# Performance work log

Measured on AMD Instinct MI355X. Metric: run time of the kernel, lower is better.

The kernel has to match this reference:

```python
import jax, jax.numpy as jnp
import numpy as np

B, H, W, C = 8, 56, 56, 384
HEADS = 12
HD = C // HEADS          # 32 head dim
WS = 7                   # window size
SS = 3                   # shift size
N = WS * WS              # 49 tokens per window
HID = int(C * 4.0)       # 1536 mlp hidden
NW = (H // WS) * (W // WS)  # 64 windows per image
EPS = 1e-5


def _relative_position_index(ws):
    coords = np.stack(np.meshgrid(np.arange(ws), np.arange(ws), indexing='ij'))
    cf = coords.reshape(2, -1)
    rel = (cf[:, :, None] - cf[:, None, :]).transpose(1, 2, 0)
    rel[:, :, 0] += ws - 1
    rel[:, :, 1] += ws - 1
    rel[:, :, 0] *= 2 * ws - 1
    return rel.sum(-1).astype(np.int32)  # [N, N]

REL_IDX = _relative_position_index(WS)


def _swin_shift_mask(hh, ww, ws, ss):
    # standard Swin shift mask: label 9 regions, windows with mixed labels get -100
    img = np.zeros((hh, ww), dtype=np.float32)
    cnt = 0
    for hs in (slice(0, -ws), slice(-ws, -ss), slice(-ss, None)):
        for wsl in (slice(0, -ws), slice(-ws, -ss), slice(-ss, None)):
            img[hs, wsl] = cnt
            cnt += 1
    wins = img.reshape(hh // ws, ws, ww // ws, ws).transpose(0, 2, 1, 3).reshape(-1, ws * ws)
    diff = wins[:, None, :] - wins[:, :, None]
    return np.where(diff != 0, -100.0, 0.0).astype(np.float32)  # [nW, N, N]


def setup_inputs() -> dict:
    key = jax.random.key(0)
    ks = jax.random.split(key, 8)
    s = 0.02
    return {
        'x': jax.random.normal(ks[0], (B, H, W, C), jnp.float32),
        'attention_mask': jnp.asarray(_swin_shift_mask(H, W, WS, SS)),
        'qkv_w': jax.random.normal(ks[1], (C, 3 * C), jnp.float32) * s,
        'qkv_b': jnp.zeros((3 * C,), jnp.float32),
        'proj_w': jax.random.normal(ks[2], (C, C), jnp.float32) * s,
        'proj_b': jnp.zeros((C,), jnp.float32),
        'rpb_table': jax.random.normal(ks[3], ((2 * WS - 1) * (2 * WS - 1), HEADS), jnp.float32) * s,
        'norm1_g': jnp.ones((C,), jnp.float32),
        'norm1_b': jnp.zeros((C,), jnp.float32),
        'norm2_g': jnp.ones((C,), jnp.float32),
        'norm2_b': jnp.zeros((C,), jnp.float32),
        'fc1_w': jax.random.normal(ks[4], (C, HID), jnp.float32) * s,
        'fc1_b': jnp.zeros((HID,), jnp.float32),
        'fc2_w': jax.random.normal(ks[5], (HID, C), jnp.float32) * s,
        'fc2_b': jnp.zeros((C,), jnp.float32),
    }


def _ln(x, g, b):
    mu = jnp.mean(x, axis=-1, keepdims=True)
    var = jnp.mean(jnp.square(x - mu), axis=-1, keepdims=True)
    return (x - mu) / jnp.sqrt(var + EPS) * g + b


def reference(x, attention_mask, qkv_w, qkv_b, proj_w, proj_b, rpb_table,
              norm1_g, norm1_b, norm2_g, norm2_b, fc1_w, fc1_b, fc2_w, fc2_b):
    b = x.shape[0]
    nh, nw = H // WS, W // WS
    shortcut = x.reshape(b, H * W, C)

    h = _ln(x, norm1_g, norm1_b)
    # cyclic shift (H,W divisible by WS -> no padding needed)
    h = jnp.roll(h, (-SS, -SS), axis=(1, 2))
    # window partition -> [b*nW, N, C]
    win = h.reshape(b, nh, WS, nw, WS, C).transpose(0, 1, 3, 2, 4, 5).reshape(-1, N, C)

    qkv = (win @ qkv_w + qkv_b).reshape(-1, N, 3, HEADS, HD).transpose(2, 0, 3, 1, 4)
    q, k, v = qkv[0] * (HD ** -0.5), qkv[1], qkv[2]  # each [b*nW, heads, N, HD]

    attn = jnp.einsum('bhnd,bhmd->bhnm', q, k)  # [b*nW, heads, N, N]
    bias = rpb_table[REL_IDX.reshape(-1)].reshape(N, N, HEADS).transpose(2, 0, 1)
    attn = attn + bias[None]
    # additive shift mask per window
    attn = attn.reshape(b, NW, HEADS, N, N) + attention_mask[None, :, None]
    attn = jax.nn.softmax(attn.reshape(-1, HEADS, N, N), axis=-1)

    out = jnp.einsum('bhnm,bhmd->bhnd', attn, v).transpose(0, 2, 1, 3).reshape(-1, N, C)
    out = out @ proj_w + proj_b
    # window reverse
    out = out.reshape(b, nh, nw, WS, WS, C).transpose(0, 1, 3, 2, 4, 5).reshape(b, H, W, C)
    out = jnp.roll(out, (SS, SS), axis=(1, 2)).reshape(b, H * W, C)

    xr = shortcut + out
    m = _ln(xr.reshape(b, H * W, C), norm2_g, norm2_b)
    m = jax.nn.gelu(m @ fc1_w + fc1_b, approximate=False) @ fc2_w + fc2_b
    xr = xr + m
    return xr.reshape(b, H, W, C)
```

## Files before the change

### kernel.cpp

```cpp
#include <hip/hip_runtime.h>
#include <hip/hip_bf16.h>
#include <math.h>

#define BD 8
#define HH 56
#define WW 56
#define CC 384
#define HEADS 12
#define HD 32
#define WS 7
#define SS 3
#define NTOK 49
#define NWIN 64
#define TOKENS (BD*HH*WW)
#define HID 1536
#define TPI (HH*WW)

typedef __attribute__((ext_vector_type(8))) short bf16x8;
typedef __attribute__((ext_vector_type(4))) float f32x4;

__device__ __forceinline__ unsigned short f2bf(float f) {
    unsigned int u = __float_as_uint(f);
    unsigned int r = (u + 0x7FFFu + ((u >> 16) & 1u)) >> 16;
    return (unsigned short)r;
}
__device__ __forceinline__ unsigned short f2bf_fast(float v) {
    unsigned int w;
    asm("v_cvt_pk_bf16_f32 %0, %1, %2" : "=v"(w) : "v"(v), "v"(v));
    return (unsigned short)w;
}
__device__ __forceinline__ float bf2f(unsigned short h) {
    return __uint_as_float(((unsigned int)h) << 16);
}
__device__ __forceinline__ void gload16(const void* g, void* l) {
    __builtin_amdgcn_global_load_lds((const __attribute__((address_space(1))) unsigned int*)g,
                                     (__attribute__((address_space(3))) unsigned int*)l, 16, 0, 0);
}
__device__ __forceinline__ float fgelu(float x) {
    float x2 = x * x;
    float y  = x * fmaf(0.03567740814f, x2, 0.7978845608f);
    float e  = exp2f(y * 2.8853900818f);
    float r  = __builtin_amdgcn_rcpf(e + 1.0f);
    return x - x * r;
}
__device__ __forceinline__ int xcd_swz(int lid, int nwg) {
    int xcd = lid & 7, pos = lid >> 3;
    int q = nwg >> 3, r = nwg & 7;
    return (xcd < r ? xcd * (q + 1) : r * (q + 1) + (xcd - r) * q) + pos;
}

__global__ __launch_bounds__(256)
void wprep(const float* __restrict__ W, unsigned short* __restrict__ Th, int K, int N)
{
    __shared__ float t[32][33];
    int n0 = blockIdx.x * 32, k0 = blockIdx.y * 32;
    int c = threadIdx.x & 31, r = threadIdx.x >> 5;
    #pragma unroll
    for (int rr = 0; rr < 32; rr += 8)
        t[r + rr][c] = W[(size_t)(k0 + r + rr) * N + n0 + c];
    __syncthreads();
    #pragma unroll
    for (int rr = 0; rr < 32; rr += 8) {
        int i = r + rr;
        Th[(size_t)(n0 + i) * K + k0 + c] = f2bf(t[c][i]);
    }
}

__global__ __launch_bounds__(256)
void bias_prep(const float* __restrict__ rpb, float* __restrict__ Bias)
{
    int e = blockIdx.x * 256 + threadIdx.x;
    int wtq = e / 49152;
    int hr  = e - wtq * 49152;
    int h   = hr >> 12;
    int rem = hr & 4095;
    int jt = rem >> 10, it = (rem >> 8) & 3, lane = (rem >> 2) & 63, reg = rem & 3;
    int j = jt * 16 + ((lane >> 4) << 2) + reg;
    int i = it * 16 + (lane & 15);
    float val;
    if (j >= NTOK) val = -1e30f;
    else if (i >= NTOK) val = 0.0f;
    else {
        int ti = i / 7, tj = i - ti * 7, yj = j / 7, xj = j - yj * 7;
        float b = rpb[((ti - yj + 6) * 13 + (tj - xj + 6)) * HEADS + h];
        int wh7 = wtq >> 1, ww7 = wtq & 1;
        int lhi = wh7 ? (ti < 4 ? 1 : 2) : 0, lhj = wh7 ? (yj < 4 ? 1 : 2) : 0;
        int lwi = ww7 ? (tj < 4 ? 1 : 2) : 0, lwj = ww7 ? (xj < 4 ? 1 : 2) : 0;
        if (lhi != lhj || lwi != lwj) b -= 100.0f;
        val = b * 5.65685424949238f;
    }
    Bias[e] = val;
}

template<bool SHIFT>
__global__ __launch_bounds__(128)
void ln_kernel(const float* __restrict__ in, const float* __restrict__ g,
               const float* __restrict__ beta, unsigned short* __restrict__ oh)
{
    int m = blockIdx.x;
    const float* src;
    size_t dbase = (size_t)m * CC;
    if (SHIFT) {
        int b  = m / (NWIN * NTOK);
        int rr = m % (NWIN * NTOK);
        int w  = rr / NTOK;
        int t  = rr % NTOK;
        int wh = w >> 3, ww = w & 7;
        int ti = t / 7,  tj = t - (t / 7) * 7;
        int hh = wh * WS + ti + SS;  if (hh >= HH) hh -= HH;
        int w2 = ww * WS + tj + SS;  if (w2 >= WW) w2 -= WW;
        src = in + ((size_t)b * TPI + hh * WW + w2) * CC;
    } else {
        src = in + (size_t)m * CC;
    }
    int tid = threadIdx.x;
    float v0 = src[tid], v1 = src[tid + 128], v2 = src[tid + 256];
    float s  = v0 + v1 + v2;
    float ss = v0*v0 + v1*v1 + v2*v2;
    #pragma unroll
    for (int off = 32; off > 0; off >>= 1) {
        s  += __shfl_down(s, off);
        ss += __shfl_down(ss, off);
    }
    __shared__ float red[4];
    int wid = tid >> 6, lane = tid & 63;
    if (lane == 0) { red[wid] = s; red[wid + 2] = ss; }
    __syncthreads();
    float tot   = red[0] + red[1];
    float totss = red[2] + red[3];
    float mu   = tot * (1.0f / CC);
    float var  = totss * (1.0f / CC) - mu * mu;
    float rstd = rsqrtf(var + 1e-5f);
    #pragma unroll
    for (int e = 0; e < 3; ++e) {
        int idx = tid + e * 128;
        float v = (e == 0 ? v0 : (e == 1 ? v1 : v2));
        float y = (v - mu) * rstd * g[idx] + beta[idx];
        oh[dbase + idx] = f2bf_fast(y);
    }
}

#define EPI_QKV  0
#define EPI_GELU 1
#define EPI_PROJ 2
#define EPI_FC2  3

template<int EPI>
__global__ __launch_bounds__(512)
void gemm_mfma(const unsigned short* __restrict__ Ah, const unsigned short* __restrict__ Bh,
               const float* __restrict__ bias, const float* __restrict__ extra,
               float* __restrict__ outf, unsigned short* __restrict__ outh,
               int M, int N, int K)
{
    __shared__ unsigned short lds[2][128][32];

    int nwg = gridDim.x * gridDim.y;
    int wid = xcd_swz(blockIdx.y * gridDim.x + blockIdx.x, nwg);
    int nblk = wid % gridDim.x;
    int mblk = wid / gridDim.x;

    int tid  = threadIdx.x;
    int lane = tid & 63;
    int wave = tid >> 6;
    int wr = wave >> 2;
    int wc = wave & 3;
    int m0 = mblk * 128, n0 = nblk * 128;

    int lrow = lane >> 2;
    int ps   = lane & 3;
    int kslot = lane >> 4;
    int rA    = lane & 15;

    const unsigned short* gsrc[2];
    unsigned short* dsts[2];
    #pragma unroll
    for (int s = 0; s < 2; ++s) {
        int seg = wave * 2 + s;
        int bf = seg >> 3, c = seg & 7;
        const unsigned short* gb = (bf == 0) ? Ah : Bh;
        int r0 = (bf == 0) ? m0 : n0;
        int row = c * 16 + lrow;
        int ks = ps ^ ((row >> 1) & 3);
        gsrc[s] = gb + (size_t)(r0 + row) * K + ks * 8;
        dsts[s] = &lds[bf][c * 16][0];
    }

    f32x4 acc[4][2];
    #pragma unroll
    for (int i = 0; i < 4; ++i)
        #pragma unroll
        for (int j = 0; j < 2; ++j)
            acc[i][j] = (f32x4){0.f, 0.f, 0.f, 0.f};

    for (int k0 = 0; k0 < K; k0 += 32) {
        #pragma unroll
        for (int s = 0; s < 2; ++s)
            gload16(gsrc[s] + k0, dsts[s]);
        __syncthreads();

        bf16x8 ah[4], bh[2];
        #pragma unroll
        for (int f = 0; f < 4; ++f) {
            int row = wr * 64 + f * 16 + rA;
            int p = (kslot ^ ((row >> 1) & 3)) * 8;
            ah[f] = *(const bf16x8*)&lds[0][row][p];
        }
        #pragma unroll
        for (int f = 0; f < 2; ++f) {
            int col = wc * 32 + f * 16 + rA;
            int pb = (kslot ^ ((col >> 1) & 3)) * 8;
            bh[f] = *(const bf16x8*)&lds[1][col][pb];
        }
        #pragma unroll
        for (int i = 0; i < 4; ++i)
            #pragma unroll
            for (int j = 0; j < 2; ++j)
                acc[i][j] = __builtin_amdgcn_mfma_f32_16x16x32_bf16(ah[i], bh[j], acc[i][j], 0, 0, 0);
        __syncthreads();
    }

    int cn = lane & 15;
    int rb = (lane >> 4) * 4;
    float bj[2];
    #pragma unroll
    for (int j = 0; j < 2; ++j) bj[j] = bias[n0 + wc * 32 + j * 16 + cn];
    int ncol = n0 + wc * 32 + cn;

    #pragma unroll
    for (int i = 0; i < 4; ++i) {
        #pragma unroll
        for (int r = 0; r < 4; ++r) {
            int mg = m0 + wr * 64 + i * 16 + rb + r;
            if (EPI == EPI_PROJ) {
                int b  = mg / (NWIN * NTOK);
                int rr = mg % (NWIN * NTOK);
                int w  = rr / NTOK;
                int t  = rr % NTOK;
                int wh = w >> 3, ww = w & 7;
                int ti = t / 7,  tj = t - (t / 7) * 7;
                int hh = wh * WS + ti + SS;  if (hh >= HH) hh -= HH;
                int w2 = ww * WS + tj + SS;  if (w2 >= WW) w2 -= WW;
                size_t pix = (size_t)b * TPI + hh * WW + w2;
                const float* xin = extra + pix * CC + ncol;
                float* xo = outf + pix * CC + ncol;
                #pragma unroll
                for (int j = 0; j < 2; ++j) xo[j * 16] = xin[j * 16] + acc[i][j][r] + bj[j];
            } else {
                const float* xi = extra + (size_t)mg * N + ncol;
                float* xo = outf + (size_t)mg * N + ncol;
                #pragma unroll
                for (int j = 0; j < 2; ++j) xo[j * 16] = xi[j * 16] + acc[i][j][r] + bj[j];
            }
        }
    }
}

template<int EPI>
__global__ __launch_bounds__(512)
void gemm_mfma256(const unsigned short* __restrict__ Ah, const unsigned short* __restrict__ Bh,
                  const float* __restrict__ bias,
                  float* __restrict__ outf, unsigned short* __restrict__ outh,
                  int M, int N, int K)
{
    __shared__ unsigned short ldsA[2][256][32];
    __shared__ unsigned short ldsB[2][128][32];

    int nwg = gridDim.x * gridDim.y;
    int wid = xcd_swz(blockIdx.y * gridDim.x + blockIdx.x, nwg);
    int nblk = wid % gridDim.x;
    int mblk = wid / gridDim.x;

    int tid  = threadIdx.x;
    int lane = tid & 63;
    int wave = tid >> 6;
    int wr = wave >> 1;
    int wc = wave & 1;
    int m0 = mblk * 256, n0 = nblk * 128;

    int lrow = lane >> 2;
    int ps   = lane & 3;
    int kslot = lane >> 4;
    int rA    = lane & 15;

    const unsigned short* gsrc[3];
    unsigned short* dst0[3];
    unsigned short* dst1[3];
    #pragma unroll
    for (int s = 0; s < 3; ++s) {
        int seg = wave * 3 + s;
        const unsigned short* gb;
        unsigned short *l0, *l1;
        int c, r0;
        if (seg < 16) { gb = Ah; c = seg;      r0 = m0; l0 = &ldsA[0][c * 16][0]; l1 = &ldsA[1][c * 16][0]; }
        else          { gb = Bh; c = seg - 16; r0 = n0; l0 = &ldsB[0][c * 16][0]; l1 = &ldsB[1][c * 16][0]; }
        int row = c * 16 + lrow;
        int ks = ps ^ ((row >> 1) & 3);
        gsrc[s] = gb + (size_t)(r0 + row) * K + ks * 8;
        dst0[s] = l0; dst1[s] = l1;
    }

    f32x4 acc[4][4];
    #pragma unroll
    for (int i = 0; i < 4; ++i)
        #pragma unroll
        for (int j = 0; j < 4; ++j)
            acc[i][j] = (f32x4){0.f, 0.f, 0.f, 0.f};

    for (int k0 = 0; k0 < K; k0 += 64) {
        #pragma unroll
        for (int s = 0; s < 3; ++s)
            gload16(gsrc[s] + k0, dst0[s]);
        #pragma unroll
        for (int s = 0; s < 3; ++s)
            gload16(gsrc[s] + k0 + 32, dst1[s]);
        __syncthreads();

        #pragma unroll
        for (int h = 0; h < 2; ++h) {
            bf16x8 ah[4], bh[4];
            #pragma unroll
            for (int f = 0; f < 4; ++f) {
                int row = wr * 64 + f * 16 + rA;
                int p = (kslot ^ ((row >> 1) & 3)) * 8;
                ah[f] = *(const bf16x8*)&ldsA[h][row][p];
                int col = wc * 64 + f * 16 + rA;
                int pb = (kslot ^ ((col >> 1) & 3)) * 8;
                bh[f] = *(const bf16x8*)&ldsB[h][col][pb];
            }
            #pragma unroll
            for (int i = 0; i < 4; ++i)
                #pragma unroll
                for (int j = 0; j < 4; ++j)
                    acc[i][j] = __builtin_amdgcn_mfma_f32_16x16x32_bf16(ah[i], bh[j], acc[i][j], 0, 0, 0);
        }
        __syncthreads();
    }

    int cn = lane & 15;
    int rb = (lane >> 4) * 4;
    float bj[4];
    #pragma unroll
    for (int j = 0; j < 4; ++j) bj[j] = bias[n0 + wc * 64 + j * 16 + cn];
    int ncol = n0 + wc * 64 + cn;

    #pragma unroll
    for (int i = 0; i < 4; ++i) {
        #pragma unroll
        for (int r = 0; r < 4; ++r) {
            int mg = m0 + wr * 64 + i * 16 + rb + r;
            if (EPI == EPI_QKV) {
                unsigned short* orow = outh + (size_t)mg * N + ncol;
                #pragma unroll
                for (int j = 0; j < 4; ++j) orow[j * 16] = f2bf_fast(acc[i][j][r] + bj[j]);
            } else {
                unsigned short* orow = outh + (size_t)mg * N + ncol;
                #pragma unroll
                for (int j = 0; j < 4; ++j)
                    orow[j * 16] = f2bf_fast(fgelu(acc[i][j][r] + bj[j]));
            }
        }
    }
}

__global__ __launch_bounds__(256)
void attn3(const unsigned short* __restrict__ QKVb, const float* __restrict__ Bias,
           unsigned short* __restrict__ outh, int win0)
{
    int wave = threadIdx.x >> 6, lane = threadIdx.x & 63;
    int unit = blockIdx.x * 4 + wave;
    int head = unit % HEADS;
    int winl = unit / HEADS;
    int wing = win0 + winl;
    int wl   = wing & (NWIN - 1);
    int wt   = (((wl >> 3) == 7) << 1) | ((wl & 7) == 7);
    int qbase = winl * NTOK;
    size_t obase = (size_t)wing * NTOK;

    __shared__ __align__(16) unsigned short Pl_all[4][64][64];
    __shared__ __align__(16) unsigned short Vt_all[4][2048];
    unsigned short (*Pl)[64] = Pl_all[wave];
    unsigned short* Vt = Vt_all[wave];

    int l15 = lane & 15, g = lane >> 4;

    for (int idx = lane; idx < 480; idx += 64) {
        int d = idx & 31, t = 49 + (idx >> 5);
        Vt[d * 64 + (((t >> 3) ^ (d & 7)) << 3) + (t & 7)] = 0;
    }
    for (int idx = lane; idx < 196; idx += 64) {
        int t = idx >> 2, c = idx & 3;
        bf16x8 v = *(const bf16x8*)(QKVb + (size_t)(qbase + t) * 1152 + 768 + head * HD + c * 8);
        int tb = t >> 3, tl = t & 7;
        #pragma unroll
        for (int e = 0; e < 8; ++e) {
            int d = c * 8 + e;
            Vt[d * 64 + ((tb ^ e) << 3) + tl] = (unsigned short)v[e];
        }
    }

    bf16x8 kf[4], qf[4];
    #pragma unroll
    for (int t = 0; t < 4; ++t) {
        int rr = t * 16 + l15; if (rr > NTOK - 1) rr = NTOK - 1;
        const unsigned short* base = QKVb + (size_t)(qbase + rr) * 1152 + head * HD + g * 8;
        qf[t] = *(const bf16x8*)base;
        kf[t] = *(const bf16x8*)(base + 384);
    }

    const float* bb = Bias + (((size_t)wt * HEADS + head) << 12);
    f32x4 acc[4][4];
    #pragma unroll
    for (int jt = 0; jt < 4; ++jt)
        #pragma unroll
        for (int it = 0; it < 4; ++it) {
            f32x4 c = *(const f32x4*)(bb + ((jt * 4 + it) * 64 + lane) * 4);
            acc[jt][it] = __builtin_amdgcn_mfma_f32_16x16x32_bf16(kf[jt], qf[it], c, 0, 0, 0);
        }

    const float K1 = 0.25503488f;
    #pragma unroll
    for (int jt = 0; jt < 4; ++jt)
        #pragma unroll
        for (int it = 0; it < 4; ++it)
            #pragma unroll
            for (int r = 0; r < 4; ++r)
                acc[jt][it][r] = exp2f(acc[jt][it][r] * K1);

    #pragma unroll
    for (int it = 0; it < 4; ++it) {
        float s = 0.0f;
        #pragma unroll
        for (int jt = 0; jt < 4; ++jt)
            s += (acc[jt][it][0] + acc[jt][it][1]) + (acc[jt][it][2] + acc[jt][it][3]);
        s += __shfl_xor(s, 16);
        s += __shfl_xor(s, 32);
        float inv = 1.0f / s;
        int i  = it * 16 + l15;
        int sw = (i & 7) << 3;
        #pragma unroll
        for (int jt = 0; jt < 4; ++jt) {
            float a0 = acc[jt][it][0] * inv, a1 = acc[jt][it][1] * inv;
            float a2 = acc[jt][it][2] * inv, a3 = acc[jt][it][3] * inv;
            unsigned int w0, w1;
            asm("v_cvt_pk_bf16_f32 %0, %1, %2" : "=v"(w0) : "v"(a0), "v"(a1));
            asm("v_cvt_pk_bf16_f32 %0, %1, %2" : "=v"(w1) : "v"(a2), "v"(a3));
            int js = (jt * 16 + g * 4) ^ sw;
            *(unsigned int*)&Pl[i][js]     = w0;
            *(unsigned int*)&Pl[i][js + 2] = w1;
        }
    }

    bf16x8 vf[2][2];
    #pragma unroll
    for (int dt = 0; dt < 2; ++dt)
        #pragma unroll
        for (int kc = 0; kc < 2; ++kc) {
            int d = dt * 16 + l15;
            vf[dt][kc] = *(const bf16x8*)&Vt[d * 64 + (((kc * 4 + g) ^ (d & 7)) << 3)];
        }
    f32x4 oacc[4][2];
    #pragma unroll
    for (int it = 0; it < 4; ++it)
        #pragma unroll
        for (int dt = 0; dt < 2; ++dt)
            oacc[it][dt] = (f32x4){0.f, 0.f, 0.f, 0.f};

    #pragma unroll
    for (int it = 0; it < 4; ++it) {
        int i  = it * 16 + l15;
        int sw = (i & 7) << 3;
        #pragma unroll
        for (int kc = 0; kc < 2; ++kc) {
            int js = (kc * 32 + g * 8) ^ sw;
            bf16x8 pf = *(const bf16x8*)&Pl[i][js];
            #pragma unroll
            for (int dt = 0; dt < 2; ++dt)
                oacc[it][dt] = __builtin_amdgcn_mfma_f32_16x16x32_bf16(pf, vf[dt][kc], oacc[it][dt], 0, 0, 0);
        }
    }

    #pragma unroll
    for (int it = 0; it < 4; ++it) {
        #pragma unroll
        for (int r = 0; r < 4; ++r) {
            int i = it * 16 + g * 4 + r;
            if (i < NTOK) {
                unsigned short* orow = outh + (obase + i) * CC + head * HD;
                orow[l15]      = f2bf_fast(oacc[it][0][r]);
                orow[16 + l15] = f2bf_fast(oacc[it][1][r]);
            }
        }
    }
}

extern "C" void kernel_launch(void* const* d_in, const int* in_sizes, int n_in,
                              void* d_out, int out_size, void* d_ws, size_t ws_size,
                              hipStream_t stream)
{
    const float* x      = (const float*)d_in[0];
    const float* qkv_w  = (const float*)d_in[2];
    const float* qkv_b  = (const float*)d_in[3];
    const float* proj_w = (const float*)d_in[4];
    const float* proj_b = (const float*)d_in[5];
    const float* rpb    = (const float*)d_in[6];
    const float* n1g    = (const float*)d_in[7];
    const float* n1b    = (const float*)d_in[8];
    const float* n2g    = (const float*)d_in[9];
    const float* n2b    = (const float*)d_in[10];
    const float* fc1w   = (const float*)d_in[11];
    const float* fc1b   = (const float*)d_in[12];
    const float* fc2w   = (const float*)d_in[13];
    const float* fc2b   = (const float*)d_in[14];

    float* xr = (float*)d_out;

    unsigned short* p = (unsigned short*)d_ws;
    unsigned short* Wqh = p; p += 442368;
    unsigned short* Wph = p; p += 147456;
    unsigned short* W1h = p; p += 589824;
    unsigned short* W2h = p; p += 589824;
    unsigned short* ABh = p; p += (size_t)TOKENS * CC;
    float* Bias = (float*)p;
    unsigned short* region = (unsigned short*)(Bias + 196608);
    unsigned short* Hbuf = region;

    const size_t FIXED = 23592960;
    size_t R = (ws_size > FIXED) ? ws_size - FIXED : 0;
    int gq = 2;
    if (R >= (size_t)8 * TPI * 1152 * 2)      gq = 8;
    else if (R >= (size_t)4 * TPI * 1152 * 2) gq = 4;
    int gh = 2;
    if (R >= (size_t)8 * TPI * HID * 2)      gh = 8;
    else if (R >= (size_t)4 * TPI * HID * 2) gh = 4;

    unsigned short* QKVb = region;

    bias_prep<<<768, 256, 0, stream>>>(rpb, Bias);
    wprep<<<dim3(1152/32, 384/32), 256, 0, stream>>>(qkv_w, Wqh, 384, 1152);
    wprep<<<dim3(384/32,  384/32), 256, 0, stream>>>(proj_w, Wph, 384, 384);
    wprep<<<dim3(1536/32, 384/32), 256, 0, stream>>>(fc1w,  W1h, 384, 1536);
    wprep<<<dim3(384/32, 1536/32), 256, 0, stream>>>(fc2w,  W2h, 1536, 384);

    ln_kernel<true><<<TOKENS, 128, 0, stream>>>(x, n1g, n1b, ABh);

    for (int c = 0; c < 8 / gq; ++c) {
        size_t off = (size_t)c * gq * TPI;
        int M = gq * TPI;
        dim3 gmm((3 * CC) / 128, M / 256);
        gemm_mfma256<EPI_QKV><<<gmm, 512, 0, stream>>>(
            ABh + off * CC, Wqh, qkv_b, nullptr, QKVb, M, 3 * CC, CC);
        attn3<<<gq * NWIN * HEADS / 4, 256, 0, stream>>>(
            QKVb, Bias, ABh, c * gq * NWIN);
    }

    {
        dim3 gmm(CC / 128, TOKENS / 128);
        gemm_mfma<EPI_PROJ><<<gmm, 512, 0, stream>>>(
            ABh, Wph, proj_b, x, xr, nullptr, TOKENS, CC, CC);
    }

    ln_kernel<false><<<TOKENS, 128, 0, stream>>>(xr, n2g, n2b, ABh);

    for (int c = 0; c < 8 / gh; ++c) {
        size_t off = (size_t)c * gh * TPI;
        int M = gh * TPI;
        {
            dim3 gmm(HID / 128, M / 256);
            gemm_mfma256<EPI_GELU><<<gmm, 512, 0, stream>>>(
                ABh + off * CC, W1h, fc1b, nullptr, Hbuf, M, HID, CC);
        }
        {
            dim3 gmm(CC / 128, M / 128);
            gemm_mfma<EPI_FC2><<<gmm, 512, 0, stream>>>(
                Hbuf, W2h, fc2b, xr + off * CC, (float*)d_out + off * CC, nullptr, M, CC, HID);
        }
    }
}
```

Baseline: 217.4 us.

## Double-buffer LDS in both MFMA GEMM kernels to overlap loads with compute

Both GEMM kernels now use two LDS stages. The global-to-LDS load for the next K-slice is issued before the MFMA compute on the current slice, so memory latency can hide behind matrix math instead of stalling at each barrier. The 128-tile kernel doubles its LDS footprint, which may lower occupancy. Correctness also depends on the gload16 (direct-to-LDS) ordering relative to the barriers.

After: 217.4 us. No clear change (+0.0%).

```diff
diff --git a/kernel.cpp b/kernel.cpp
--- a/kernel.cpp
+++ b/kernel.cpp
@@ -145,6 +145,27 @@
 #define EPI_PROJ 2
 #define EPI_FC2  3
 
+#define COMPUTE128(B) do {                                                          \
+    bf16x8 ah[4], bh[2];                                                            \
+    _Pragma("unroll")                                                               \
+    for (int f = 0; f < 4; ++f) {                                                   \
+        int row = wr * 64 + f * 16 + rA;                                            \
+        int pp = (kslot ^ ((row >> 1) & 3)) * 8;                                    \
+        ah[f] = *(const bf16x8*)&lds[B][0][row][pp];                                \
+    }                                                                               \
+    _Pragma("unroll")                                                               \
+    for (int f = 0; f < 2; ++f) {                                                   \
+        int col = wc * 32 + f * 16 + rA;                                            \
+        int pb = (kslot ^ ((col >> 1) & 3)) * 8;                                    \
+        bh[f] = *(const bf16x8*)&lds[B][1][col][pb];                                \
+    }                                                                               \
+    _Pragma("unroll")                                                               \
+    for (int i = 0; i < 4; ++i)                                                     \
+        _Pragma("unroll")                                                           \
+        for (int j = 0; j < 2; ++j)                                                 \
+            acc[i][j] = __builtin_amdgcn_mfma_f32_16x16x32_bf16(ah[i], bh[j], acc[i][j], 0, 0, 0); \
+} while (0)
+
 template<int EPI>
 __global__ __launch_bounds__(512)
 void gemm_mfma(const unsigned short* __restrict__ Ah, const unsigned short* __restrict__ Bh,
@@ -152,7 +173,7 @@
                float* __restrict__ outf, unsigned short* __restrict__ outh,
                int M, int N, int K)
 {
-    __shared__ unsigned short lds[2][128][32];
+    __shared__ unsigned short lds[2][2][128][32];
 
     int nwg = gridDim.x * gridDim.y;
     int wid = xcd_swz(blockIdx.y * gridDim.x + blockIdx.x, nwg);
@@ -172,7 +193,8 @@
     int rA    = lane & 15;
 
     const unsigned short* gsrc[2];
-    unsigned short* dsts[2];
+    unsigned short* d0[2];
+    unsigned short* d1[2];
     #pragma unroll
     for (int s = 0; s < 2; ++s) {
         int seg = wave * 2 + s;
@@ -182,7 +204,8 @@
         int row = c * 16 + lrow;
         int ks = ps ^ ((row >> 1) & 3);
         gsrc[s] = gb + (size_t)(r0 + row) * K + ks * 8;
-        dsts[s] = &lds[bf][c * 16][0];
+        d0[s] = &lds[0][bf][c * 16][0];
+        d1[s] = &lds[1][bf][c * 16][0];
     }
 
     f32x4 acc[4][2];
@@ -192,30 +215,24 @@
         for (int j = 0; j < 2; ++j)
             acc[i][j] = (f32x4){0.f, 0.f, 0.f, 0.f};
 
-    for (int k0 = 0; k0 < K; k0 += 32) {
-        #pragma unroll
-        for (int s = 0; s < 2; ++s)
-            gload16(gsrc[s] + k0, dsts[s]);
+    const int nt = K / 32;
+    gload16(gsrc[0], d0[0]);
+    gload16(gsrc[1], d0[1]);
+    __syncthreads();
+    for (int t = 0; t < nt; t += 2) {
+        {
+            int k1 = (t + 1) * 32;
+            gload16(gsrc[0] + k1, d1[0]);
+            gload16(gsrc[1] + k1, d1[1]);
+        }
+        COMPUTE128(0);
         __syncthreads();
-
-        bf16x8 ah[4], bh[2];
-        #pragma unroll
-        for (int f = 0; f < 4; ++f) {
-            int row = wr * 64 + f * 16 + rA;
-            int p = (kslot ^ ((row >> 1) & 3)) * 8;
-            ah[f] = *(const bf16x8*)&lds[0][row][p];
-        }
-        #pragma unroll
-        for (int f = 0; f < 2; ++f) {
-            int col = wc * 32 + f * 16 + rA;
-            int pb = (kslot ^ ((col >> 1) & 3)) * 8;
-            bh[f] = *(const bf16x8*)&lds[1][col][pb];
-        }
-        #pragma unroll
-        for (int i = 0; i < 4; ++i)
-            #pragma unroll
-            for (int j = 0; j < 2; ++j)
-                acc[i][j] = __builtin_amdgcn_mfma_f32_16x16x32_bf16(ah[i], bh[j], acc[i][j], 0, 0, 0);
+        if (t + 2 < nt) {
+            int k2 = (t + 2) * 32;
+            gload16(gsrc[0] + k2, d0[0]);
+            gload16(gsrc[1] + k2, d0[1]);
+        }
+        COMPUTE128(1);
         __syncthreads();
     }
 
@@ -255,6 +272,24 @@
     }
 }
 
+#define COMPUTE256(B) do {                                                          \
+    bf16x8 ah[4], bh[4];                                                            \
+    _Pragma("unroll")                                                               \
+    for (int f = 0; f < 4; ++f) {                                                   \
+        int row = wr * 64 + f * 16 + rA;                                            \
+        int pp = (kslot ^ ((row >> 1) & 3)) * 8;                                    \
+        ah[f] = *(const bf16x8*)&ldsA[B][row][pp];                                  \
+        int col = wc * 64 + f * 16 + rA;                                            \
+        int pb = (kslot ^ ((col >> 1) & 3)) * 8;                                    \
+        bh[f] = *(const bf16x8*)&ldsB[B][col][pb];                                  \
+    }                                                                               \
+    _Pragma("unroll")                                                               \
+    for (int i = 0; i < 4; ++i)                                                     \
+        _Pragma("unroll")                                                           \
+        for (int j = 0; j < 4; ++j)                                                 \
+            acc[i][j] = __builtin_amdgcn_mfma_f32_16x16x32_bf16(ah[i], bh[j], acc[i][j], 0, 0, 0); \
+} while (0)
+
 template<int EPI>
 __global__ __launch_bounds__(512)
 void gemm_mfma256(const unsigned short* __restrict__ Ah, const unsigned short* __restrict__ Bh,
@@ -283,8 +318,8 @@
     int rA    = lane & 15;
 
     const unsigned short* gsrc[3];
-    unsigned short* dst0[3];
-    unsigned short* dst1[3];
+    unsigned short* d0[3];
+    unsigned short* d1[3];
     #pragma unroll
     for (int s = 0; s < 3; ++s) {
         int seg = wave * 3 + s;
@@ -296,7 +331,7 @@
         int row = c * 16 + lrow;
         int ks = ps ^ ((row >> 1) & 3);
         gsrc[s] = gb + (size_t)(r0 + row) * K + ks * 8;
-        dst0[s] = l0; dst1[s] = l1;
+        d0[s] = l0; d1[s] = l1;
     }
 
     f32x4 acc[4][4];
@@ -306,33 +341,24 @@
         for (int j = 0; j < 4; ++j)
             acc[i][j] = (f32x4){0.f, 0.f, 0.f, 0.f};
 
-    for (int k0 = 0; k0 < K; k0 += 64) {
-        #pragma unroll
-        for (int s = 0; s < 3; ++s)
-            gload16(gsrc[s] + k0, dst0[s]);
-        #pragma unroll
-        for (int s = 0; s < 3; ++s)
-            gload16(gsrc[s] + k0 + 32, dst1[s]);
+    const int nt = K / 32;
+    #pragma unroll
+    for (int s = 0; s < 3; ++s) gload16(gsrc[s], d0[s]);
+    __syncthreads();
+    for (int t = 0; t < nt; t += 2) {
+        {
+            int k1 = (t + 1) * 32;
+            #pragma unroll
+            for (int s = 0; s < 3; ++s) gload16(gsrc[s] + k1, d1[s]);
+        }
+        COMPUTE256(0);
         __syncthreads();
-
-        #pragma unroll
-        for (int h = 0; h < 2; ++h) {
-            bf16x8 ah[4], bh[4];
+        if (t + 2 < nt) {
+            int k2 = (t + 2) * 32;
             #pragma unroll
-            for (int f = 0; f < 4; ++f) {
-                int row = wr * 64 + f * 16 + rA;
-                int p = (kslot ^ ((row >> 1) & 3)) * 8;
-                ah[f] = *(const bf16x8*)&ldsA[h][row][p];
-                int col = wc * 64 + f * 16 + rA;
-                int pb = (kslot ^ ((col >> 1) & 3)) * 8;
-                bh[f] = *(const bf16x8*)&ldsB[h][col][pb];
-            }
-            #pragma unroll
-            for (int i = 0; i < 4; ++i)
-                #pragma unroll
-                for (int j = 0; j < 4; ++j)
-                    acc[i][j] = __builtin_amdgcn_mfma_f32_16x16x32_bf16(ah[i], bh[j], acc[i][j], 0, 0, 0);
-        }
+            for (int s = 0; s < 3; ++s) gload16(gsrc[s] + k2, d0[s]);
+        }
+        COMPUTE256(1);
         __syncthreads();
     }
 
```
